# Performance work log

Measured on AMD Instinct MI355X. Metric: run time of the kernel, lower is better.

The kernel has to match this reference:

```python
import jax, jax.numpy as jnp
import numpy as np

EPS_BN = 1e-5


def _batchnorm(h, g, b):
    # training-mode BatchNorm1d over the flattened (B*N*k) axis
    mu = jnp.mean(h, axis=0)
    var = jnp.var(h, axis=0)
    return g * (h - mu) * jax.lax.rsqrt(var + EPS_BN) + b


def setup_inputs() -> dict:
    key = jax.random.key(0)
    ks = jax.random.split(key, 5)
    B, N = 4, 8192
    x = jax.random.normal(ks[0], (B, N, 3), dtype=jnp.float32)
    W1 = jax.random.normal(ks[1], (7, 10), dtype=jnp.float32) * (1.0 / np.sqrt(7.0))
    b1 = jax.random.normal(ks[2], (10,), dtype=jnp.float32) * 0.01
    W2 = jax.random.normal(ks[3], (10, 10), dtype=jnp.float32) * (1.0 / np.sqrt(10.0))
    b2 = jax.random.normal(ks[4], (10,), dtype=jnp.float32) * 0.01
    g1 = jnp.ones((10,), jnp.float32); be1 = jnp.zeros((10,), jnp.float32)
    g2 = jnp.ones((10,), jnp.float32); be2 = jnp.zeros((10,), jnp.float32)
    return {"x": x, "W1": W1, "b1": b1, "g1": g1, "be1": be1,
            "W2": W2, "b2": b2, "g2": g2, "be2": be2, "k": 9}


def reference(x, W1, b1, g1, be1, W2, b2, g2, be2, k):
    B, N, C = x.shape
    # --- kNN graph (brute force, self included as nearest) ---
    sq = jnp.sum(x * x, axis=-1)                                    # (B,N)
    d2 = sq[:, :, None] + sq[:, None, :] - 2.0 * jnp.einsum('bnc,bmc->bnm', x, x)
    _, idx = jax.lax.top_k(-d2, k + 1)                              # (B,N,k+1)
    nbrs = x[jnp.arange(B)[:, None, None], idx]                     # (B,N,k+1,3)
    rel = (nbrs - x[:, :, None, :])[:, :, 1:, :]                    # drop self -> (B,N,k,3)
    # --- sort neighbors by azimuth phi = atan2(y, x) ---
    phi = jnp.arctan2(rel[..., 1], rel[..., 0])                     # (B,N,k)
    order = jnp.argsort(phi, axis=-1)
    v1 = jnp.take_along_axis(rel, order[..., None], axis=2)         # (B,N,k,3)
    v2 = jnp.roll(v1, -1, axis=2)                                   # next neighbor (cyclic)
    # --- umbrella-style surface features ---
    centroids = 0.5 * (v1 + v2)
    normals = jnp.cross(v1, v2)
    normals = normals / (jnp.linalg.norm(normals, axis=-1, keepdims=True) + 1e-6)
    sign = jnp.where(normals[..., 0:1, 0] > 0, 1.0, -1.0)[..., None]  # (B,N,1,1)
    normals = normals * sign
    position = jnp.sum(normals * centroids, axis=-1, keepdims=True) / jnp.sqrt(jnp.asarray(3.0, x.dtype))
    feat = jnp.concatenate([centroids, normals, position], axis=-1)   # (B,N,k,7)
    feat = feat.reshape(B * N * k, 7)
    # --- tiny MLP + max-pool over k ---
    h = jax.nn.relu(_batchnorm(feat @ W1 + b1, g1, be1))
    h = jax.nn.relu(_batchnorm(h @ W2 + b2, g2, be2))
    return jnp.max(h.reshape(B, N, k, 10), axis=2)                  # (B,N,10)
```

## Files before the change

kernel.cpp:

```cpp
#include <hip/hip_runtime.h>
#include <math.h>
#include <float.h>
#include <stdint.h>

#define B_ 4
#define N_ 8192
#define K_ 9
#define NPTS (B_ * N_)
#define NROWS (NPTS * K_)
#define SPLIT 8
#define CHUNK (N_ / SPLIT)
#define NGROUP 32
#define GSIZE (CHUNK / NGROUP)
#define GSTRIDE 33
#define NCOPY 16

typedef float f4 __attribute__((ext_vector_type(4)));
typedef float f32x2 __attribute__((ext_vector_type(2)));

__device__ __forceinline__ f32x2 dist2_pk(f32x2 xx, f32x2 yy, f32x2 zz, f32x2 ww,
                                          f32x2 qx, f32x2 qy, f32x2 qz, f32x2 qw) {
  f32x2 t0 = qx * xx;
  f32x2 t1 = __builtin_elementwise_fma(qy, yy, t0);
  f32x2 t2 = __builtin_elementwise_fma(qz, zz, t1);
  f32x2 s  = qw + ww;
  f32x2 m2 = {-2.0f, -2.0f};
  return __builtin_elementwise_fma(t2, m2, s);
}

#define GDECL(G) float gd##G; int gi##G;
#define TOURN8()                                                           \
  float e01d, e23d, e45d, e67d, f03d, f47d, md;                            \
  int   e01i, e23i, e45i, e67i, f03i, f47i, mi;                            \
  { bool t;                                                                \
    t = d1 < d0; e01d = t ? d1 : d0; e01i = t ? (j + 1) : (j + 0);         \
    t = d3 < d2; e23d = t ? d3 : d2; e23i = t ? (j + 3) : (j + 2);         \
    t = d5 < d4; e45d = t ? d5 : d4; e45i = t ? (j + 5) : (j + 4);         \
    t = d7 < d6; e67d = t ? d7 : d6; e67i = t ? (j + 7) : (j + 6);         \
    t = e23d < e01d; f03d = t ? e23d : e01d; f03i = t ? e23i : e01i;       \
    t = e67d < e45d; f47d = t ? e67d : e45d; f47i = t ? e67i : e45i;       \
    t = f47d < f03d; md = t ? f47d : f03d; mi = t ? f47i : f03i; }
#define SCANG(G)                                                           \
  { float bgd = FLT_MAX; int bgi = 0;                                      \
    _Pragma("clang loop unroll(disable)")                                  \
    for (int pr = 0; pr < 16; pr += 4) {                                   \
      const f4* cp = CH + (G * GSTRIDE + 2 * pr);                          \
      f4 A0 = cp[0], B0 = cp[1], A1 = cp[2], B1 = cp[3];                   \
      f4 A2 = cp[4], B2 = cp[5], A3 = cp[6], B3 = cp[7];                   \
      int j = G * GSIZE + 2 * pr;                                          \
      f32x2 dA = dist2_pk(__builtin_shufflevector(A0, A0, 0, 1),           \
                          __builtin_shufflevector(A0, A0, 2, 3),           \
                          __builtin_shufflevector(B0, B0, 0, 1),           \
                          __builtin_shufflevector(B0, B0, 2, 3),           \
                          qx2, qy2, qz2, qw2);                             \
      f32x2 dB = dist2_pk(__builtin_shufflevector(A1, A1, 0, 1),           \
                          __builtin_shufflevector(A1, A1, 2, 3),           \
                          __builtin_shufflevector(B1, B1, 0, 1),           \
                          __builtin_shufflevector(B1, B1, 2, 3),           \
                          qx2, qy2, qz2, qw2);                             \
      f32x2 dC = dist2_pk(__builtin_shufflevector(A2, A2, 0, 1),           \
                          __builtin_shufflevector(A2, A2, 2, 3),           \
                          __builtin_shufflevector(B2, B2, 0, 1),           \
                          __builtin_shufflevector(B2, B2, 2, 3),           \
                          qx2, qy2, qz2, qw2);                             \
      f32x2 dD = dist2_pk(__builtin_shufflevector(A3, A3, 0, 1),           \
                          __builtin_shufflevector(A3, A3, 2, 3),           \
                          __builtin_shufflevector(B3, B3, 0, 1),           \
                          __builtin_shufflevector(B3, B3, 2, 3),           \
                          qx2, qy2, qz2, qw2);                             \
      float d0 = dA.x, d1 = dA.y, d2 = dB.x, d3 = dB.y;                    \
      float d4 = dC.x, d5 = dC.y, d6 = dD.x, d7 = dD.y;                    \
      if (HS) {                                                            \
        d0 = (j + 0 == nl) ? FLT_MAX : d0;                                 \
        d1 = (j + 1 == nl) ? FLT_MAX : d1;                                 \
        d2 = (j + 2 == nl) ? FLT_MAX : d2;                                 \
        d3 = (j + 3 == nl) ? FLT_MAX : d3;                                 \
        d4 = (j + 4 == nl) ? FLT_MAX : d4;                                 \
        d5 = (j + 5 == nl) ? FLT_MAX : d5;                                 \
        d6 = (j + 6 == nl) ? FLT_MAX : d6;                                 \
        d7 = (j + 7 == nl) ? FLT_MAX : d7;                                 \
      }                                                                    \
      TOURN8();                                                            \
      bool lt = md < bgd; bgd = lt ? md : bgd; bgi = lt ? mi : bgi;        \
    }                                                                      \
    gd##G = bgd; gi##G = bgi; }
#define LMC(G, S)                                                          \
  { bool lt = gd##G < wd##S;                                               \
    wd##S = lt ? gd##G : wd##S; wi##S = lt ? gi##G : wi##S;                \
    wg##S = lt ? G : wg##S; }
#define CMB(S)                                                             \
  { bool lt = wd##S < wda;                                                 \
    wda = lt ? wd##S : wda; wia = lt ? wi##S : wia; wga = lt ? wg##S : wga; }
#define WBK(G)                                                             \
  { bool m = (wg == G); gd##G = m ? nd : gd##G; gi##G = m ? ni : gi##G; }

template <bool HS>
__device__ __forceinline__ void knn_chunk(const f4* CH, f32x2 qx2, f32x2 qy2,
                                          f32x2 qz2, f32x2 qw2,
                                          int nl, int j0, int s, int p,
                                          uint2* __restrict__ PBDI) {
  GDECL(0) GDECL(1) GDECL(2) GDECL(3) GDECL(4) GDECL(5) GDECL(6) GDECL(7)
  GDECL(8) GDECL(9) GDECL(10) GDECL(11) GDECL(12) GDECL(13) GDECL(14) GDECL(15)
  GDECL(16) GDECL(17) GDECL(18) GDECL(19) GDECL(20) GDECL(21) GDECL(22) GDECL(23)
  GDECL(24) GDECL(25) GDECL(26) GDECL(27) GDECL(28) GDECL(29) GDECL(30) GDECL(31)

  SCANG(0) SCANG(1) SCANG(2) SCANG(3) SCANG(4) SCANG(5) SCANG(6) SCANG(7)
  SCANG(8) SCANG(9) SCANG(10) SCANG(11) SCANG(12) SCANG(13) SCANG(14) SCANG(15)
  SCANG(16) SCANG(17) SCANG(18) SCANG(19) SCANG(20) SCANG(21) SCANG(22) SCANG(23)
  SCANG(24) SCANG(25) SCANG(26) SCANG(27) SCANG(28) SCANG(29) SCANG(30) SCANG(31)

#pragma clang loop unroll(disable)
  for (int r = 0; r < K_; ++r) {
    float wda = gd0; int wia = gi0; int wga = 0;
    LMC(1,a) LMC(2,a) LMC(3,a) LMC(4,a) LMC(5,a) LMC(6,a) LMC(7,a)
    float wdb = gd8; int wib = gi8; int wgb = 8;
    LMC(9,b) LMC(10,b) LMC(11,b) LMC(12,b) LMC(13,b) LMC(14,b) LMC(15,b)
    float wdc = gd16; int wic = gi16; int wgc = 16;
    LMC(17,c) LMC(18,c) LMC(19,c) LMC(20,c) LMC(21,c) LMC(22,c) LMC(23,c)
    float wdd = gd24; int wid = gi24; int wgd = 24;
    LMC(25,d) LMC(26,d) LMC(27,d) LMC(28,d) LMC(29,d) LMC(30,d) LMC(31,d)
    CMB(b) CMB(c) CMB(d)
    float wd = wda; int wi = wia; int wg = wga;

    uint2 o; o.x = __float_as_uint(wd); o.y = (unsigned)(j0 + wi);
    PBDI[(size_t)(s * K_ + r) * NPTS + p] = o;

    int ab = wg * GSTRIDE;
    int jb = wg * GSIZE;
    float nd = FLT_MAX; int ni = 0;
#pragma clang loop unroll(disable)
    for (int pr = 0; pr < 16; pr += 4) {
      const f4* cp = CH + (ab + 2 * pr);
      f4 A0 = cp[0], B0 = cp[1], A1 = cp[2], B1 = cp[3];
      f4 A2 = cp[4], B2 = cp[5], A3 = cp[6], B3 = cp[7];
      int j = jb + 2 * pr;
      f32x2 dA = dist2_pk(__builtin_shufflevector(A0, A0, 0, 1),
                          __builtin_shufflevector(A0, A0, 2, 3),
                          __builtin_shufflevector(B0, B0, 0, 1),
                          __builtin_shufflevector(B0, B0, 2, 3),
                          qx2, qy2, qz2, qw2);
      f32x2 dB = dist2_pk(__builtin_shufflevector(A1, A1, 0, 1),
                          __builtin_shufflevector(A1, A1, 2, 3),
                          __builtin_shufflevector(B1, B1, 0, 1),
                          __builtin_shufflevector(B1, B1, 2, 3),
                          qx2, qy2, qz2, qw2);
      f32x2 dC = dist2_pk(__builtin_shufflevector(A2, A2, 0, 1),
                          __builtin_shufflevector(A2, A2, 2, 3),
                          __builtin_shufflevector(B2, B2, 0, 1),
                          __builtin_shufflevector(B2, B2, 2, 3),
                          qx2, qy2, qz2, qw2);
      f32x2 dD = dist2_pk(__builtin_shufflevector(A3, A3, 0, 1),
                          __builtin_shufflevector(A3, A3, 2, 3),
                          __builtin_shufflevector(B3, B3, 0, 1),
                          __builtin_shufflevector(B3, B3, 2, 3),
                          qx2, qy2, qz2, qw2);
      float d0 = dA.x, d1 = dA.y, d2 = dB.x, d3 = dB.y;
      float d4 = dC.x, d5 = dC.y, d6 = dD.x, d7 = dD.y;
      if (HS) {
        d0 = (j + 0 == nl) ? FLT_MAX : d0;
        d1 = (j + 1 == nl) ? FLT_MAX : d1;
        d2 = (j + 2 == nl) ? FLT_MAX : d2;
        d3 = (j + 3 == nl) ? FLT_MAX : d3;
        d4 = (j + 4 == nl) ? FLT_MAX : d4;
        d5 = (j + 5 == nl) ? FLT_MAX : d5;
        d6 = (j + 6 == nl) ? FLT_MAX : d6;
        d7 = (j + 7 == nl) ? FLT_MAX : d7;
      }
      bool k0 = (d0 > wd) | ((d0 == wd) & ((j + 0) > wi));
      bool k1 = (d1 > wd) | ((d1 == wd) & ((j + 1) > wi));
      bool k2 = (d2 > wd) | ((d2 == wd) & ((j + 2) > wi));
      bool k3 = (d3 > wd) | ((d3 == wd) & ((j + 3) > wi));
      bool k4 = (d4 > wd) | ((d4 == wd) & ((j + 4) > wi));
      bool k5 = (d5 > wd) | ((d5 == wd) & ((j + 5) > wi));
      bool k6 = (d6 > wd) | ((d6 == wd) & ((j + 6) > wi));
      bool k7 = (d7 > wd) | ((d7 == wd) & ((j + 7) > wi));
      d0 = k0 ? d0 : FLT_MAX;
      d1 = k1 ? d1 : FLT_MAX;
      d2 = k2 ? d2 : FLT_MAX;
      d3 = k3 ? d3 : FLT_MAX;
      d4 = k4 ? d4 : FLT_MAX;
      d5 = k5 ? d5 : FLT_MAX;
      d6 = k6 ? d6 : FLT_MAX;
      d7 = k7 ? d7 : FLT_MAX;
      TOURN8();
      bool lt = md < nd; nd = lt ? md : nd; ni = lt ? mi : ni;
    }
    WBK(0) WBK(1) WBK(2) WBK(3) WBK(4) WBK(5) WBK(6) WBK(7)
    WBK(8) WBK(9) WBK(10) WBK(11) WBK(12) WBK(13) WBK(14) WBK(15)
    WBK(16) WBK(17) WBK(18) WBK(19) WBK(20) WBK(21) WBK(22) WBK(23)
    WBK(24) WBK(25) WBK(26) WBK(27) WBK(28) WBK(29) WBK(30) WBK(31)
  }
}

__launch_bounds__(128, 4)
__global__ void k_knn(const float* __restrict__ x, uint2* __restrict__ PBDI) {
  __shared__ f4 CH[NGROUP * GSTRIDE];
  int bid = blockIdx.x;
  int pg = bid >> 3;
  int s = bid & (SPLIT - 1);
  int p = pg * 128 + threadIdx.x;
  int b = p >> 13;
  int n = p & (N_ - 1);
  int bO = b * N_;
  int j0 = s * CHUNK;

  const float* xq = x + 3 * (size_t)p;
  float qa = xq[0], qb = xq[1], qc = xq[2];
  float qw = qa * qa + qb * qb + qc * qc;
  f32x2 qx2 = {qa, qa}, qy2 = {qb, qb}, qz2 = {qc, qc}, qw2 = {qw, qw};

  for (int u = threadIdx.x; u < CHUNK / 2; u += 128) {
    const float* xp = x + 3 * (size_t)(bO + j0 + 2 * u);
    float a0 = xp[0], b0 = xp[1], c0 = xp[2];
    float a1 = xp[3], b1 = xp[4], c1 = xp[5];
    int G = u >> 4, rr = u & 15;
    f4 lo = {a0, a1, b0, b1};
    f4 hi = {c0, c1, a0 * a0 + b0 * b0 + c0 * c0, a1 * a1 + b1 * b1 + c1 * c1};
    CH[G * GSTRIDE + 2 * rr] = lo;
    CH[G * GSTRIDE + 2 * rr + 1] = hi;
  }
  __syncthreads();

  int n0 = (pg * 128) & (N_ - 1);
  int nl = n - j0;
  if (s == (n0 >> 10)) knn_chunk<true >(CH, qx2, qy2, qz2, qw2, nl, j0, s, p, PBDI);
  else                 knn_chunk<false>(CH, qx2, qy2, qz2, qw2, nl, j0, s, p, PBDI);
}

#define LVL(bdv, biv)                                                     \
  { bool lt = cd < (bdv); float td = (bdv); int ti = (biv);               \
    (bdv) = lt ? cd : (bdv); (biv) = lt ? ci : (biv);                     \
    cd = lt ? td : cd; ci = lt ? ti : ci; }
#define INS9ALL()                                                         \
  LVL(b0d, b0i) LVL(b1d, b1i) LVL(b2d, b2i) LVL(b3d, b3i) LVL(b4d, b4i)  \
  LVL(b5d, b5i) LVL(b6d, b6i) LVL(b7d, b7i) LVL(b8d, b8i)
#define TOP9_DECL()                                                       \
  float b0d = FLT_MAX, b1d = FLT_MAX, b2d = FLT_MAX, b3d = FLT_MAX,       \
        b4d = FLT_MAX, b5d = FLT_MAX, b6d = FLT_MAX, b7d = FLT_MAX,       \
        b8d = FLT_MAX;                                                    \
  int b0i = 0, b1i = 0, b2i = 0, b3i = 0, b4i = 0, b5i = 0, b6i = 0,      \
      b7i = 0, b8i = 0;

#define MKREL(T)                                                          \
  float rx##T, ry##T, rz##T, ph##T;                                       \
  { const float* mp = x + 3 * (size_t)(bO + b##T##i);                     \
    rx##T = mp[0] - qa; ry##T = mp[1] - qb; rz##T = mp[2] - qc;           \
    ph##T = atan2f(ry##T, rx##T); }

#define CE(A, Bv)                                                         \
  { bool lt = ph##Bv < ph##A; float t0;                                   \
    t0 = ph##A; ph##A = lt ? ph##Bv : t0; ph##Bv = lt ? t0 : ph##Bv;      \
    t0 = rx##A; rx##A = lt ? rx##Bv : t0; rx##Bv = lt ? t0 : rx##Bv;      \
    t0 = ry##A; ry##A = lt ? ry##Bv : t0; ry##Bv = lt ? t0 : ry##Bv;      \
    t0 = rz##A; rz##A = lt ? rz##Bv : t0; rz##Bv = lt ? t0 : rz##Bv; }

#define ST9(arr, v0, v1, v2, v3, v4, v5, v6, v7, v8)                      \
  arr[0 * 64 + pl] = v0; arr[1 * 64 + pl] = v1; arr[2 * 64 + pl] = v2;    \
  arr[3 * 64 + pl] = v3; arr[4 * 64 + pl] = v4; arr[5 * 64 + pl] = v5;    \
  arr[6 * 64 + pl] = v6; arr[7 * 64 + pl] = v7; arr[8 * 64 + pl] = v8;

__launch_bounds__(256, 4)
__global__ void k_tail1(const float* __restrict__ x, const uint2* __restrict__ PBDI,
                        const float* __restrict__ W1, const float* __restrict__ b1,
                        float* __restrict__ H1, double* __restrict__ ACC) {
  __shared__ float  LMD[64 * 37];
  __shared__ int    LMI[64 * 37];
  __shared__ float  LREL[3][9 * 64];
  __shared__ float  LSGN[64];
  __shared__ double sred[4][20];

  int q = threadIdx.x >> 6;
  int pl = threadIdx.x & 63;
  int pbase = blockIdx.x * 64;
  int p = pbase + pl;

  {
    TOP9_DECL();
#pragma clang loop unroll_count(2)
    for (int e = 0; e < 2 * K_; ++e) {
      uint2 v = PBDI[(size_t)(q * 2 * K_ + e) * NPTS + p];
      float cd = __uint_as_float(v.x);
      int ci = (int)v.y;
      INS9ALL();
    }
    int base = pl * 37 + q * 9;
    LMD[base + 0] = b0d; LMD[base + 1] = b1d; LMD[base + 2] = b2d;
    LMD[base + 3] = b3d; LMD[base + 4] = b4d; LMD[base + 5] = b5d;
    LMD[base + 6] = b6d; LMD[base + 7] = b7d; LMD[base + 8] = b8d;
    LMI[base + 0] = b0i; LMI[base + 1] = b1i; LMI[base + 2] = b2i;
    LMI[base + 3] = b3i; LMI[base + 4] = b4i; LMI[base + 5] = b5i;
    LMI[base + 6] = b6i; LMI[base + 7] = b7i; LMI[base + 8] = b8i;
  }
  __syncthreads();

  if (q == 0) {
    int b = p >> 13;
    int bO = b * N_;
    const float* xq = x + 3 * (size_t)p;
    float qa = xq[0], qb = xq[1], qc = xq[2];

    TOP9_DECL();
#pragma clang loop unroll_count(3)
    for (int e = 0; e < 4 * K_; ++e) {
      float cd = LMD[pl * 37 + e];
      int ci = LMI[pl * 37 + e];
      INS9ALL();
    }

    MKREL(0) MKREL(1) MKREL(2) MKREL(3) MKREL(4)
    MKREL(5) MKREL(6) MKREL(7) MKREL(8)

    CE(0,1)
    CE(1,2) CE(0,1)
    CE(2,3) CE(1,2) CE(0,1)
    CE(3,4) CE(2,3) CE(1,2) CE(0,1)
    CE(4,5) CE(3,4) CE(2,3) CE(1,2) CE(0,1)
    CE(5,6) CE(4,5) CE(3,4) CE(2,3) CE(1,2) CE(0,1)
    CE(6,7) CE(5,6) CE(4,5) CE(3,4) CE(2,3) CE(1,2) CE(0,1)
    CE(7,8) CE(6,7) CE(5,6) CE(4,5) CE(3,4) CE(2,3) CE(1,2) CE(0,1)

    float nx0 = ry0 * rz1 - rz0 * ry1;
    float ny0 = rz0 * rx1 - rx0 * rz1;
    float nz0 = rx0 * ry1 - ry0 * rx1;
    float nrm0 = sqrtf(nx0 * nx0 + ny0 * ny0 + nz0 * nz0) + 1e-6f;
    LSGN[pl] = ((nx0 / nrm0) > 0.0f) ? 1.0f : -1.0f;

    ST9(LREL[0], rx0, rx1, rx2, rx3, rx4, rx5, rx6, rx7, rx8)
    ST9(LREL[1], ry0, ry1, ry2, ry3, ry4, ry5, ry6, ry7, ry8)
    ST9(LREL[2], rz0, rz1, rz2, rz3, rz4, rz5, rz6, rz7, rz8)
  }
  __syncthreads();

  double sum[10], ss[10];
#pragma unroll
  for (int c = 0; c < 10; ++c) { sum[c] = 0.0; ss[c] = 0.0; }

#pragma clang loop unroll(disable)
  for (int rl = threadIdx.x; rl < 9 * 64; rl += 256) {
    int t = rl >> 6;
    int pp = rl & 63;
    int t2 = (t + 1 == K_) ? 0 : t + 1;
    float v1x = LREL[0][t * 64 + pp];
    float v1y = LREL[1][t * 64 + pp];
    float v1z = LREL[2][t * 64 + pp];
    float v2x = LREL[0][t2 * 64 + pp];
    float v2y = LREL[1][t2 * 64 + pp];
    float v2z = LREL[2][t2 * 64 + pp];
    float sgn = LSGN[pp];

    float cx = 0.5f * (v1x + v2x);
    float cy = 0.5f * (v1y + v2y);
    float cz = 0.5f * (v1z + v2z);
    float nx = v1y * v2z - v1z * v2y;
    float ny = v1z * v2x - v1x * v2z;
    float nz = v1x * v2y - v1y * v2x;
    float nrm = sqrtf(nx * nx + ny * ny + nz * nz) + 1e-6f;
    nx /= nrm; ny /= nrm; nz /= nrm;
    nx *= sgn; ny *= sgn; nz *= sgn;
    float pos = (nx * cx + ny * cy + nz * cz) / 1.7320508075688772f;

    float fv[7] = {cx, cy, cz, nx, ny, nz, pos};
#pragma unroll
    for (int c = 0; c < 10; ++c) {
      float h = b1[c];
#pragma unroll
      for (int rr = 0; rr < 7; ++rr) h = fmaf(fv[rr], W1[rr * 10 + c], h);
      H1[(size_t)c * NROWS + (size_t)t * NPTS + pbase + pp] = h;
      double hd = (double)h;
      sum[c] += hd; ss[c] += hd * hd;
    }
  }

  int lane = threadIdx.x & 63, wv = threadIdx.x >> 6;
#pragma unroll
  for (int c = 0; c < 10; ++c) {
    double a = sum[c];
#pragma unroll
    for (int off = 32; off > 0; off >>= 1) a += __shfl_down(a, off);
    if (lane == 0) sred[wv][c] = a;
    double qq = ss[c];
#pragma unroll
    for (int off = 32; off > 0; off >>= 1) qq += __shfl_down(qq, off);
    if (lane == 0) sred[wv][10 + c] = qq;
  }
  __syncthreads();
  if (threadIdx.x < 20) {
    atomicAdd(&ACC[(blockIdx.x & (NCOPY - 1)) * 40 + threadIdx.x],
              sred[0][threadIdx.x] + sred[1][threadIdx.x] +
              sred[2][threadIdx.x] + sred[3][threadIdx.x]);
  }
}

__launch_bounds__(64)
__global__ void k_mlp2(const float* __restrict__ H1, double* __restrict__ ACC,
                       const float* __restrict__ g1, const float* __restrict__ be1,
                       const float* __restrict__ W2, const float* __restrict__ b2,
                       const float* __restrict__ g2, float* __restrict__ EXT) {
  __shared__ float MR[20];
  __shared__ double sred[20];
  if (threadIdx.x < 20) {
    int c = threadIdx.x % 10;
    int half = threadIdx.x / 10;
    double s0 = 0.0, s1 = 0.0;
#pragma unroll
    for (int cc = 0; cc < NCOPY; ++cc) {
      s0 += ACC[cc * 40 + c];
      s1 += ACC[cc * 40 + 10 + c];
    }
    double mu = s0 / (double)NROWS;
    double var = s1 / (double)NROWS - mu * mu;
    MR[threadIdx.x] = half ? (float)(1.0 / sqrt(var + 1e-5)) : (float)mu;
  }
  __syncthreads();

  int p = blockIdx.x * 64 + threadIdx.x;
  double sum[10], ss[10];
  float ext[10], sg[10];
#pragma unroll
  for (int c = 0; c < 10; ++c) {
    sum[c] = 0.0; ss[c] = 0.0;
    sg[c] = g2[c];
    ext[c] = (sg[c] >= 0.0f) ? -FLT_MAX : FLT_MAX;
  }

#pragma clang loop unroll(disable)
  for (int t = 0; t < K_; ++t) {
    float v[10];
#pragma unroll
    for (int c = 0; c < 10; ++c) {
      float h = H1[(size_t)c * NROWS + (size_t)t * NPTS + p];
      float z = g1[c] * (h - MR[c]) * MR[10 + c] + be1[c];
      v[c] = z > 0.0f ? z : 0.0f;
    }
#pragma unroll
    for (int c = 0; c < 10; ++c) {
      float h = b2[c];
#pragma unroll
      for (int u = 0; u < 10; ++u) h = fmaf(v[u], W2[u * 10 + c], h);
      sum[c] += (double)h;
      ss[c] += (double)h * (double)h;
      ext[c] = (sg[c] >= 0.0f) ? fmaxf(ext[c], h) : fminf(ext[c], h);
    }
  }

#pragma unroll
  for (int c = 0; c < 10; ++c)
    EXT[(size_t)c * NPTS + p] = ext[c];

#pragma unroll
  for (int c = 0; c < 10; ++c) {
    double a = sum[c];
#pragma unroll
    for (int off = 32; off > 0; off >>= 1) a += __shfl_down(a, off);
    if (threadIdx.x == 0) sred[c] = a;
    double qq = ss[c];
#pragma unroll
    for (int off = 32; off > 0; off >>= 1) qq += __shfl_down(qq, off);
    if (threadIdx.x == 0) sred[10 + c] = qq;
  }
  __syncthreads();
  if (threadIdx.x < 20) {
    atomicAdd(&ACC[(blockIdx.x & (NCOPY - 1)) * 40 + 20 + threadIdx.x],
              sred[threadIdx.x]);
  }
}

__launch_bounds__(64)
__global__ void k_out(const float* __restrict__ EXT, const double* __restrict__ ACC,
                      const float* __restrict__ g2, const float* __restrict__ be2,
                      float* __restrict__ out) {
  __shared__ float MR[20];
  if (threadIdx.x < 20) {
    int c = threadIdx.x % 10;
    int half = threadIdx.x / 10;
    double s0 = 0.0, s1 = 0.0;
#pragma unroll
    for (int cc = 0; cc < NCOPY; ++cc) {
      s0 += ACC[cc * 40 + 20 + c];
      s1 += ACC[cc * 40 + 30 + c];
    }
    double mu = s0 / (double)NROWS;
    double var = s1 / (double)NROWS - mu * mu;
    MR[threadIdx.x] = half ? (float)(1.0 / sqrt(var + 1e-5)) : (float)mu;
  }
  __syncthreads();

  int p = blockIdx.x * 64 + threadIdx.x;
#pragma unroll
  for (int c = 0; c < 10; ++c) {
    float h = EXT[(size_t)c * NPTS + p];
    float z = g2[c] * (h - MR[c]) * MR[10 + c] + be2[c];
    z = z > 0.0f ? z : 0.0f;
    out[(size_t)p * 10 + c] = z;
  }
}

extern "C" void kernel_launch(void* const* d_in, const int* in_sizes, int n_in,
                              void* d_out, int out_size, void* d_ws, size_t ws_size,
                              hipStream_t stream) {
  (void)in_sizes; (void)n_in; (void)out_size; (void)ws_size;
  const float* x  = (const float*)d_in[0];
  const float* W1 = (const float*)d_in[1];
  const float* b1 = (const float*)d_in[2];
  const float* g1 = (const float*)d_in[3];
  const float* be1= (const float*)d_in[4];
  const float* W2 = (const float*)d_in[5];
  const float* b2 = (const float*)d_in[6];
  const float* g2 = (const float*)d_in[7];
  const float* be2= (const float*)d_in[8];
  float* out = (float*)d_out;

  char* base = (char*)d_ws;
  uint2*  PBDI = (uint2*)base;
  float*  H1 = (float*)(base + (size_t)SPLIT * K_ * NPTS * 8);
  double* ACC = (double*)(H1 + (size_t)10 * NROWS);
  float*  EXT = (float*)PBDI;

  hipMemsetAsync(ACC, 0, NCOPY * 40 * sizeof(double), stream);
  k_knn<<<(NPTS / 128) * SPLIT, 128, 0, stream>>>(x, PBDI);
  k_tail1<<<NPTS / 64, 256, 0, stream>>>(x, PBDI, W1, b1, H1, ACC);
  k_mlp2<<<NPTS / 64, 64, 0, stream>>>(H1, ACC, g1, be1, W2, b2, g2, EXT);
  k_out<<<NPTS / 64, 64, 0, stream>>>(EXT, ACC, g2, be2, out);
}
```

Measured before the change: 231.6 us.

## Process two query points per thread in kNN scan and defer index recovery

Each thread now handles two query points, so every LDS load of candidate points is reused for two distance computations. The initial per-group scan keeps only the min distance and which 8-wide sub-block held it, using fminf. The exact index is recovered lazily during extraction by recomputing that sub-block. The ACC memset is folded into block 0 of the kNN kernel, and launch bounds drop to 2 waves/SIMD, which raises register pressure and halves the grid size.

```diff
diff --git a/kernel.cpp b/kernel.cpp
--- a/kernel.cpp
+++ b/kernel.cpp
@@ -18,6 +18,8 @@
 typedef float f4 __attribute__((ext_vector_type(4)));
 typedef float f32x2 __attribute__((ext_vector_type(2)));
 
+#define SH2(V, a, b) __builtin_shufflevector(V, V, a, b)
+
 __device__ __forceinline__ f32x2 dist2_pk(f32x2 xx, f32x2 yy, f32x2 zz, f32x2 ww,
                                           f32x2 qx, f32x2 qy, f32x2 qz, f32x2 qw) {
   f32x2 t0 = qx * xx;
@@ -28,7 +30,69 @@
   return __builtin_elementwise_fma(t2, m2, s);
 }
 
-#define GDECL(G) float gd##G; int gi##G;
+#define WLOAD(cp)                                                          \
+  f4 A0 = (cp)[0], B0 = (cp)[1], A1 = (cp)[2], B1 = (cp)[3],               \
+     A2 = (cp)[4], B2 = (cp)[5], A3 = (cp)[6], B3 = (cp)[7];
+
+#define WDIST(QX, QY, QZ, QW)                                              \
+  f32x2 dP0 = dist2_pk(SH2(A0,0,1), SH2(A0,2,3), SH2(B0,0,1), SH2(B0,2,3), \
+                       QX, QY, QZ, QW);                                    \
+  f32x2 dP1 = dist2_pk(SH2(A1,0,1), SH2(A1,2,3), SH2(B1,0,1), SH2(B1,2,3), \
+                       QX, QY, QZ, QW);                                    \
+  f32x2 dP2 = dist2_pk(SH2(A2,0,1), SH2(A2,2,3), SH2(B2,0,1), SH2(B2,2,3), \
+                       QX, QY, QZ, QW);                                    \
+  f32x2 dP3 = dist2_pk(SH2(A3,0,1), SH2(A3,2,3), SH2(B3,0,1), SH2(B3,2,3), \
+                       QX, QY, QZ, QW);                                    \
+  float d0 = dP0.x, d1 = dP0.y, d2 = dP1.x, d3 = dP1.y;                    \
+  float d4 = dP2.x, d5 = dP2.y, d6 = dP3.x, d7 = dP3.y;
+
+#define HSMASK(JV, NL)                                                     \
+  if (HS) {                                                                \
+    d0 = ((JV) + 0 == (NL)) ? FLT_MAX : d0;                                \
+    d1 = ((JV) + 1 == (NL)) ? FLT_MAX : d1;                                \
+    d2 = ((JV) + 2 == (NL)) ? FLT_MAX : d2;                                \
+    d3 = ((JV) + 3 == (NL)) ? FLT_MAX : d3;                                \
+    d4 = ((JV) + 4 == (NL)) ? FLT_MAX : d4;                                \
+    d5 = ((JV) + 5 == (NL)) ? FLT_MAX : d5;                                \
+    d6 = ((JV) + 6 == (NL)) ? FLT_MAX : d6;                                \
+    d7 = ((JV) + 7 == (NL)) ? FLT_MAX : d7;                                \
+  }
+
+#define FMIN8 fminf(fminf(fminf(d0, d1), fminf(d2, d3)),                   \
+                    fminf(fminf(d4, d5), fminf(d6, d7)))
+
+#define GDECL2(G) float gdA##G; int giA##G; float gdB##G; int giB##G;
+
+#define SCANG2(G)                                                          \
+  { float bgdA = FLT_MAX; int bqA = 0;                                     \
+    float bgdB = FLT_MAX; int bqB = 0;                                     \
+    _Pragma("clang loop unroll(disable)")                                  \
+    for (int pr = 0; pr < 16; pr += 4) {                                   \
+      const f4* cp = CH + (G * GSTRIDE + 2 * pr);                          \
+      WLOAD(cp)                                                            \
+      int j = G * GSIZE + 2 * pr;                                          \
+      { WDIST(qx2A, qy2A, qz2A, qw2A)                                      \
+        HSMASK(j, nlA)                                                     \
+        float m = FMIN8;                                                   \
+        bool lt = m < bgdA; bgdA = lt ? m : bgdA; bqA = lt ? pr : bqA; }   \
+      { WDIST(qx2B, qy2B, qz2B, qw2B)                                      \
+        HSMASK(j, nlB)                                                     \
+        float m = FMIN8;                                                   \
+        bool lt = m < bgdB; bgdB = lt ? m : bgdB; bqB = lt ? pr : bqB; }   \
+    }                                                                      \
+    gdA##G = bgdA; giA##G = -1 - bqA;                                      \
+    gdB##G = bgdB; giB##G = -1 - bqB; }
+
+#define LMQ(G, S, Q)                                                       \
+  { bool lt = gd##Q##G < wd##S;                                            \
+    wd##S = lt ? gd##Q##G : wd##S; wi##S = lt ? gi##Q##G : wi##S;          \
+    wg##S = lt ? G : wg##S; }
+#define CMBQ(S)                                                            \
+  { bool lt = wd##S < wda;                                                 \
+    wda = lt ? wd##S : wda; wia = lt ? wi##S : wia; wga = lt ? wg##S : wga; }
+#define WBKQ(G, Q)                                                         \
+  { bool m = (wg == G); gd##Q##G = m ? nd : gd##Q##G;                      \
+    gi##Q##G = m ? ni : gi##Q##G; }
 #define TOURN8()                                                           \
   float e01d, e23d, e45d, e67d, f03d, f47d, md;                            \
   int   e01i, e23i, e45i, e67i, f03i, f47i, mi;                            \
@@ -40,174 +104,143 @@
     t = e23d < e01d; f03d = t ? e23d : e01d; f03i = t ? e23i : e01i;       \
     t = e67d < e45d; f47d = t ? e67d : e45d; f47i = t ? e67i : e45i;       \
     t = f47d < f03d; md = t ? f47d : f03d; mi = t ? f47i : f03i; }
-#define SCANG(G)                                                           \
-  { float bgd = FLT_MAX; int bgi = 0;                                      \
+
+#define EXTRACTLOOP(Q)                                                     \
+  _Pragma("clang loop unroll(disable)")                                    \
+  for (int r = 0; r < K_; ++r) {                                           \
+    float wda = gd##Q##0; int wia = gi##Q##0; int wga = 0;                 \
+    LMQ(1,a,Q) LMQ(2,a,Q) LMQ(3,a,Q) LMQ(4,a,Q) LMQ(5,a,Q) LMQ(6,a,Q)     \
+    LMQ(7,a,Q)                                                             \
+    float wdb = gd##Q##8; int wib = gi##Q##8; int wgb = 8;                 \
+    LMQ(9,b,Q) LMQ(10,b,Q) LMQ(11,b,Q) LMQ(12,b,Q) LMQ(13,b,Q)            \
+    LMQ(14,b,Q) LMQ(15,b,Q)                                                \
+    float wdc = gd##Q##16; int wic = gi##Q##16; int wgc = 16;              \
+    LMQ(17,c,Q) LMQ(18,c,Q) LMQ(19,c,Q) LMQ(20,c,Q) LMQ(21,c,Q)           \
+    LMQ(22,c,Q) LMQ(23,c,Q)                                                \
+    float wdd = gd##Q##24; int wid = gi##Q##24; int wgd = 24;              \
+    LMQ(25,d,Q) LMQ(26,d,Q) LMQ(27,d,Q) LMQ(28,d,Q) LMQ(29,d,Q)           \
+    LMQ(30,d,Q) LMQ(31,d,Q)                                                \
+    CMBQ(b) CMBQ(c) CMBQ(d)                                                \
+    float wd = wda; int wist = wia; int wg = wga;                          \
+    int ab = wg * GSTRIDE;                                                 \
+    int jb = wg * GSIZE;                                                   \
+    int wi;                                                                \
+    { int bq = (wist >= 0) ? 0 : (-1 - wist);                              \
+      const f4* cp = CH + (ab + 2 * bq);                                   \
+      WLOAD(cp)                                                            \
+      int j = jb + 2 * bq;                                                 \
+      WDIST(qx2, qy2, qz2, qw2)                                            \
+      HSMASK(j, nl)                                                        \
+      const int IMX = 0x7fffffff;                                          \
+      int a0_ = (d0 == wd) ? (j + 0) : IMX;                                \
+      int a1_ = (d1 == wd) ? (j + 1) : IMX;                                \
+      int a2_ = (d2 == wd) ? (j + 2) : IMX;                                \
+      int a3_ = (d3 == wd) ? (j + 3) : IMX;                                \
+      int a4_ = (d4 == wd) ? (j + 4) : IMX;                                \
+      int a5_ = (d5 == wd) ? (j + 5) : IMX;                                \
+      int a6_ = (d6 == wd) ? (j + 6) : IMX;                                \
+      int a7_ = (d7 == wd) ? (j + 7) : IMX;                                \
+      int m01 = a0_ < a1_ ? a0_ : a1_;                                     \
+      int m23 = a2_ < a3_ ? a2_ : a3_;                                     \
+      int m45 = a4_ < a5_ ? a4_ : a5_;                                     \
+      int m67 = a6_ < a7_ ? a6_ : a7_;                                     \
+      int mA_ = m01 < m23 ? m01 : m23;                                     \
+      int mB_ = m45 < m67 ? m45 : m67;                                     \
+      int jm = mA_ < mB_ ? mA_ : mB_;                                      \
+      wi = (wist >= 0) ? wist : jm; }                                      \
+    uint2 o; o.x = __float_as_uint(wd); o.y = (unsigned)(j0 + wi);         \
+    PBDI[(size_t)(s * K_ + r) * NPTS + p] = o;                             \
+    float nd = FLT_MAX; int ni = 0;                                        \
     _Pragma("clang loop unroll(disable)")                                  \
     for (int pr = 0; pr < 16; pr += 4) {                                   \
-      const f4* cp = CH + (G * GSTRIDE + 2 * pr);                          \
-      f4 A0 = cp[0], B0 = cp[1], A1 = cp[2], B1 = cp[3];                   \
-      f4 A2 = cp[4], B2 = cp[5], A3 = cp[6], B3 = cp[7];                   \
-      int j = G * GSIZE + 2 * pr;                                          \
-      f32x2 dA = dist2_pk(__builtin_shufflevector(A0, A0, 0, 1),           \
-                          __builtin_shufflevector(A0, A0, 2, 3),           \
-                          __builtin_shufflevector(B0, B0, 0, 1),           \
-                          __builtin_shufflevector(B0, B0, 2, 3),           \
-                          qx2, qy2, qz2, qw2);                             \
-      f32x2 dB = dist2_pk(__builtin_shufflevector(A1, A1, 0, 1),           \
-                          __builtin_shufflevector(A1, A1, 2, 3),           \
-                          __builtin_shufflevector(B1, B1, 0, 1),           \
-                          __builtin_shufflevector(B1, B1, 2, 3),           \
-                          qx2, qy2, qz2, qw2);                             \
-      f32x2 dC = dist2_pk(__builtin_shufflevector(A2, A2, 0, 1),           \
-                          __builtin_shufflevector(A2, A2, 2, 3),           \
-                          __builtin_shufflevector(B2, B2, 0, 1),           \
-                          __builtin_shufflevector(B2, B2, 2, 3),           \
-                          qx2, qy2, qz2, qw2);                             \
-      f32x2 dD = dist2_pk(__builtin_shufflevector(A3, A3, 0, 1),           \
-                          __builtin_shufflevector(A3, A3, 2, 3),           \
-                          __builtin_shufflevector(B3, B3, 0, 1),           \
-                          __builtin_shufflevector(B3, B3, 2, 3),           \
-                          qx2, qy2, qz2, qw2);                             \
-      float d0 = dA.x, d1 = dA.y, d2 = dB.x, d3 = dB.y;                    \
-      float d4 = dC.x, d5 = dC.y, d6 = dD.x, d7 = dD.y;                    \
-      if (HS) {                                                            \
-        d0 = (j + 0 == nl) ? FLT_MAX : d0;                                 \
-        d1 = (j + 1 == nl) ? FLT_MAX : d1;                                 \
-        d2 = (j + 2 == nl) ? FLT_MAX : d2;                                 \
-        d3 = (j + 3 == nl) ? FLT_MAX : d3;                                 \
-        d4 = (j + 4 == nl) ? FLT_MAX : d4;                                 \
-        d5 = (j + 5 == nl) ? FLT_MAX : d5;                                 \
-        d6 = (j + 6 == nl) ? FLT_MAX : d6;                                 \
-        d7 = (j + 7 == nl) ? FLT_MAX : d7;                                 \
-      }                                                                    \
+      const f4* cp = CH + (ab + 2 * pr);                                   \
+      WLOAD(cp)                                                            \
+      int j = jb + 2 * pr;                                                 \
+      WDIST(qx2, qy2, qz2, qw2)                                            \
+      HSMASK(j, nl)                                                        \
+      bool k0 = (d0 > wd) | ((d0 == wd) & ((j + 0) > wi));                 \
+      bool k1 = (d1 > wd) | ((d1 == wd) & ((j + 1) > wi));                 \
+      bool k2 = (d2 > wd) | ((d2 == wd) & ((j + 2) > wi));                 \
+      bool k3 = (d3 > wd) | ((d3 == wd) & ((j + 3) > wi));                 \
+      bool k4 = (d4 > wd) | ((d4 == wd) & ((j + 4) > wi));                 \
+      bool k5 = (d5 > wd) | ((d5 == wd) & ((j + 5) > wi));                 \
+      bool k6 = (d6 > wd) | ((d6 == wd) & ((j + 6) > wi));                 \
+      bool k7 = (d7 > wd) | ((d7 == wd) & ((j + 7) > wi));                 \
+      d0 = k0 ? d0 : FLT_MAX;                                              \
+      d1 = k1 ? d1 : FLT_MAX;                                              \
+      d2 = k2 ? d2 : FLT_MAX;                                              \
+      d3 = k3 ? d3 : FLT_MAX;                                              \
+      d4 = k4 ? d4 : FLT_MAX;                                              \
+      d5 = k5 ? d5 : FLT_MAX;                                              \
+      d6 = k6 ? d6 : FLT_MAX;                                              \
+      d7 = k7 ? d7 : FLT_MAX;                                              \
       TOURN8();                                                            \
-      bool lt = md < bgd; bgd = lt ? md : bgd; bgi = lt ? mi : bgi;        \
+      bool lt = md < nd; nd = lt ? md : nd; ni = lt ? mi : ni;             \
     }                                                                      \
-    gd##G = bgd; gi##G = bgi; }
-#define LMC(G, S)                                                          \
-  { bool lt = gd##G < wd##S;                                               \
-    wd##S = lt ? gd##G : wd##S; wi##S = lt ? gi##G : wi##S;                \
-    wg##S = lt ? G : wg##S; }
-#define CMB(S)                                                             \
-  { bool lt = wd##S < wda;                                                 \
-    wda = lt ? wd##S : wda; wia = lt ? wi##S : wia; wga = lt ? wg##S : wga; }
-#define WBK(G)                                                             \
-  { bool m = (wg == G); gd##G = m ? nd : gd##G; gi##G = m ? ni : gi##G; }
+    WBKQ(0,Q) WBKQ(1,Q) WBKQ(2,Q) WBKQ(3,Q) WBKQ(4,Q) WBKQ(5,Q)           \
+    WBKQ(6,Q) WBKQ(7,Q) WBKQ(8,Q) WBKQ(9,Q) WBKQ(10,Q) WBKQ(11,Q)         \
+    WBKQ(12,Q) WBKQ(13,Q) WBKQ(14,Q) WBKQ(15,Q) WBKQ(16,Q) WBKQ(17,Q)     \
+    WBKQ(18,Q) WBKQ(19,Q) WBKQ(20,Q) WBKQ(21,Q) WBKQ(22,Q) WBKQ(23,Q)     \
+    WBKQ(24,Q) WBKQ(25,Q) WBKQ(26,Q) WBKQ(27,Q) WBKQ(28,Q) WBKQ(29,Q)     \
+    WBKQ(30,Q) WBKQ(31,Q)                                                  \
+  }
 
 template <bool HS>
-__device__ __forceinline__ void knn_chunk(const f4* CH, f32x2 qx2, f32x2 qy2,
-                                          f32x2 qz2, f32x2 qw2,
-                                          int nl, int j0, int s, int p,
-                                          uint2* __restrict__ PBDI) {
-  GDECL(0) GDECL(1) GDECL(2) GDECL(3) GDECL(4) GDECL(5) GDECL(6) GDECL(7)
-  GDECL(8) GDECL(9) GDECL(10) GDECL(11) GDECL(12) GDECL(13) GDECL(14) GDECL(15)
-  GDECL(16) GDECL(17) GDECL(18) GDECL(19) GDECL(20) GDECL(21) GDECL(22) GDECL(23)
-  GDECL(24) GDECL(25) GDECL(26) GDECL(27) GDECL(28) GDECL(29) GDECL(30) GDECL(31)
-
-  SCANG(0) SCANG(1) SCANG(2) SCANG(3) SCANG(4) SCANG(5) SCANG(6) SCANG(7)
-  SCANG(8) SCANG(9) SCANG(10) SCANG(11) SCANG(12) SCANG(13) SCANG(14) SCANG(15)
-  SCANG(16) SCANG(17) SCANG(18) SCANG(19) SCANG(20) SCANG(21) SCANG(22) SCANG(23)
-  SCANG(24) SCANG(25) SCANG(26) SCANG(27) SCANG(28) SCANG(29) SCANG(30) SCANG(31)
-
-#pragma clang loop unroll(disable)
-  for (int r = 0; r < K_; ++r) {
-    float wda = gd0; int wia = gi0; int wga = 0;
-    LMC(1,a) LMC(2,a) LMC(3,a) LMC(4,a) LMC(5,a) LMC(6,a) LMC(7,a)
-    float wdb = gd8; int wib = gi8; int wgb = 8;
-    LMC(9,b) LMC(10,b) LMC(11,b) LMC(12,b) LMC(13,b) LMC(14,b) LMC(15,b)
-    float wdc = gd16; int wic = gi16; int wgc = 16;
-    LMC(17,c) LMC(18,c) LMC(19,c) LMC(20,c) LMC(21,c) LMC(22,c) LMC(23,c)
-    float wdd = gd24; int wid = gi24; int wgd = 24;
-    LMC(25,d) LMC(26,d) LMC(27,d) LMC(28,d) LMC(29,d) LMC(30,d) LMC(31,d)
-    CMB(b) CMB(c) CMB(d)
-    float wd = wda; int wi = wia; int wg = wga;
-
-    uint2 o; o.x = __float_as_uint(wd); o.y = (unsigned)(j0 + wi);
-    PBDI[(size_t)(s * K_ + r) * NPTS + p] = o;
-
-    int ab = wg * GSTRIDE;
-    int jb = wg * GSIZE;
-    float nd = FLT_MAX; int ni = 0;
-#pragma clang loop unroll(disable)
-    for (int pr = 0; pr < 16; pr += 4) {
-      const f4* cp = CH + (ab + 2 * pr);
-      f4 A0 = cp[0], B0 = cp[1], A1 = cp[2], B1 = cp[3];
-      f4 A2 = cp[4], B2 = cp[5], A3 = cp[6], B3 = cp[7];
-      int j = jb + 2 * pr;
-      f32x2 dA = dist2_pk(__builtin_shufflevector(A0, A0, 0, 1),
-                          __builtin_shufflevector(A0, A0, 2, 3),
-                          __builtin_shufflevector(B0, B0, 0, 1),
-                          __builtin_shufflevector(B0, B0, 2, 3),
-                          qx2, qy2, qz2, qw2);
-      f32x2 dB = dist2_pk(__builtin_shufflevector(A1, A1, 0, 1),
-                          __builtin_shufflevector(A1, A1, 2, 3),
-                          __builtin_shufflevector(B1, B1, 0, 1),
-                          __builtin_shufflevector(B1, B1, 2, 3),
-                          qx2, qy2, qz2, qw2);
-      f32x2 dC = dist2_pk(__builtin_shufflevector(A2, A2, 0, 1),
-                          __builtin_shufflevector(A2, A2, 2, 3),
-                          __builtin_shufflevector(B2, B2, 0, 1),
-                          __builtin_shufflevector(B2, B2, 2, 3),
-                          qx2, qy2, qz2, qw2);
-      f32x2 dD = dist2_pk(__builtin_shufflevector(A3, A3, 0, 1),
-                          __builtin_shufflevector(A3, A3, 2, 3),
-                          __builtin_shufflevector(B3, B3, 0, 1),
-                          __builtin_shufflevector(B3, B3, 2, 3),
-                          qx2, qy2, qz2, qw2);
-      float d0 = dA.x, d1 = dA.y, d2 = dB.x, d3 = dB.y;
-      float d4 = dC.x, d5 = dC.y, d6 = dD.x, d7 = dD.y;
-      if (HS) {
-        d0 = (j + 0 == nl) ? FLT_MAX : d0;
-        d1 = (j + 1 == nl) ? FLT_MAX : d1;
-        d2 = (j + 2 == nl) ? FLT_MAX : d2;
-        d3 = (j + 3 == nl) ? FLT_MAX : d3;
-        d4 = (j + 4 == nl) ? FLT_MAX : d4;
-        d5 = (j + 5 == nl) ? FLT_MAX : d5;
-        d6 = (j + 6 == nl) ? FLT_MAX : d6;
-        d7 = (j + 7 == nl) ? FLT_MAX : d7;
-      }
-      bool k0 = (d0 > wd) | ((d0 == wd) & ((j + 0) > wi));
-      bool k1 = (d1 > wd) | ((d1 == wd) & ((j + 1) > wi));
-      bool k2 = (d2 > wd) | ((d2 == wd) & ((j + 2) > wi));
-      bool k3 = (d3 > wd) | ((d3 == wd) & ((j + 3) > wi));
-      bool k4 = (d4 > wd) | ((d4 == wd) & ((j + 4) > wi));
-      bool k5 = (d5 > wd) | ((d5 == wd) & ((j + 5) > wi));
-      bool k6 = (d6 > wd) | ((d6 == wd) & ((j + 6) > wi));
-      bool k7 = (d7 > wd) | ((d7 == wd) & ((j + 7) > wi));
-      d0 = k0 ? d0 : FLT_MAX;
-      d1 = k1 ? d1 : FLT_MAX;
-      d2 = k2 ? d2 : FLT_MAX;
-      d3 = k3 ? d3 : FLT_MAX;
-      d4 = k4 ? d4 : FLT_MAX;
-      d5 = k5 ? d5 : FLT_MAX;
-      d6 = k6 ? d6 : FLT_MAX;
-      d7 = k7 ? d7 : FLT_MAX;
-      TOURN8();
-      bool lt = md < nd; nd = lt ? md : nd; ni = lt ? mi : ni;
-    }
-    WBK(0) WBK(1) WBK(2) WBK(3) WBK(4) WBK(5) WBK(6) WBK(7)
-    WBK(8) WBK(9) WBK(10) WBK(11) WBK(12) WBK(13) WBK(14) WBK(15)
-    WBK(16) WBK(17) WBK(18) WBK(19) WBK(20) WBK(21) WBK(22) WBK(23)
-    WBK(24) WBK(25) WBK(26) WBK(27) WBK(28) WBK(29) WBK(30) WBK(31)
-  }
-}
-
-__launch_bounds__(128, 4)
-__global__ void k_knn(const float* __restrict__ x, uint2* __restrict__ PBDI) {
+__device__ __forceinline__ void knn_chunk2(
+    const f4* CH,
+    f32x2 qx2A, f32x2 qy2A, f32x2 qz2A, f32x2 qw2A,
+    f32x2 qx2B, f32x2 qy2B, f32x2 qz2B, f32x2 qw2B,
+    int nlA, int nlB, int j0, int s, int p0, int p1,
+    uint2* __restrict__ PBDI) {
+  GDECL2(0) GDECL2(1) GDECL2(2) GDECL2(3) GDECL2(4) GDECL2(5) GDECL2(6)
+  GDECL2(7) GDECL2(8) GDECL2(9) GDECL2(10) GDECL2(11) GDECL2(12) GDECL2(13)
+  GDECL2(14) GDECL2(15) GDECL2(16) GDECL2(17) GDECL2(18) GDECL2(19)
+  GDECL2(20) GDECL2(21) GDECL2(22) GDECL2(23) GDECL2(24) GDECL2(25)
+  GDECL2(26) GDECL2(27) GDECL2(28) GDECL2(29) GDECL2(30) GDECL2(31)
+
+  SCANG2(0) SCANG2(1) SCANG2(2) SCANG2(3) SCANG2(4) SCANG2(5) SCANG2(6)
+  SCANG2(7) SCANG2(8) SCANG2(9) SCANG2(10) SCANG2(11) SCANG2(12) SCANG2(13)
+  SCANG2(14) SCANG2(15) SCANG2(16) SCANG2(17) SCANG2(18) SCANG2(19)
+  SCANG2(20) SCANG2(21) SCANG2(22) SCANG2(23) SCANG2(24) SCANG2(25)
+  SCANG2(26) SCANG2(27) SCANG2(28) SCANG2(29) SCANG2(30) SCANG2(31)
+
+  {
+    f32x2 qx2 = qx2A, qy2 = qy2A, qz2 = qz2A, qw2 = qw2A;
+    int nl = nlA; int p = p0;
+    EXTRACTLOOP(A)
+  }
+  {
+    f32x2 qx2 = qx2B, qy2 = qy2B, qz2 = qz2B, qw2 = qw2B;
+    int nl = nlB; int p = p1;
+    EXTRACTLOOP(B)
+  }
+}
+
+__launch_bounds__(128, 2)
+__global__ void k_knn(const float* __restrict__ x, uint2* __restrict__ PBDI,
+                      double* __restrict__ ACC) {
   __shared__ f4 CH[NGROUP * GSTRIDE];
   int bid = blockIdx.x;
+  if (bid == 0) {
+    for (int t = threadIdx.x; t < NCOPY * 40; t += 128) ACC[t] = 0.0;
+  }
   int pg = bid >> 3;
   int s = bid & (SPLIT - 1);
-  int p = pg * 128 + threadIdx.x;
-  int b = p >> 13;
-  int n = p & (N_ - 1);
+  int pbase = pg * 256;
+  int p0 = pbase + threadIdx.x;
+  int p1 = p0 + 128;
+  int b = p0 >> 13;
   int bO = b * N_;
   int j0 = s * CHUNK;
 
-  const float* xq = x + 3 * (size_t)p;
-  float qa = xq[0], qb = xq[1], qc = xq[2];
-  float qw = qa * qa + qb * qb + qc * qc;
-  f32x2 qx2 = {qa, qa}, qy2 = {qb, qb}, qz2 = {qc, qc}, qw2 = {qw, qw};
+  const float* xq0 = x + 3 * (size_t)p0;
+  float qa0 = xq0[0], qb0 = xq0[1], qc0 = xq0[2];
+  float qw0 = qa0 * qa0 + qb0 * qb0 + qc0 * qc0;
+  const float* xq1 = x + 3 * (size_t)p1;
+  float qa1 = xq1[0], qb1 = xq1[1], qc1 = xq1[2];
+  float qw1 = qa1 * qa1 + qb1 * qb1 + qc1 * qc1;
+  f32x2 qx2A = {qa0, qa0}, qy2A = {qb0, qb0}, qz2A = {qc0, qc0}, qw2A = {qw0, qw0};
+  f32x2 qx2B = {qa1, qa1}, qy2B = {qb1, qb1}, qz2B = {qc1, qc1}, qw2B = {qw1, qw1};
 
   for (int u = threadIdx.x; u < CHUNK / 2; u += 128) {
     const float* xp = x + 3 * (size_t)(bO + j0 + 2 * u);
@@ -221,10 +254,15 @@
   }
   __syncthreads();
 
-  int n0 = (pg * 128) & (N_ - 1);
-  int nl = n - j0;
-  if (s == (n0 >> 10)) knn_chunk<true >(CH, qx2, qy2, qz2, qw2, nl, j0, s, p, PBDI);
-  else                 knn_chunk<false>(CH, qx2, qy2, qz2, qw2, nl, j0, s, p, PBDI);
+  int n0 = pbase & (N_ - 1);
+  int nlA = (n0 + threadIdx.x) - j0;
+  int nlB = nlA + 128;
+  if (s == (n0 >> 10))
+    knn_chunk2<true >(CH, qx2A, qy2A, qz2A, qw2A, qx2B, qy2B, qz2B, qw2B,
+                      nlA, nlB, j0, s, p0, p1, PBDI);
+  else
+    knn_chunk2<false>(CH, qx2A, qy2A, qz2A, qw2A, qx2B, qy2B, qz2B, qw2B,
+                      nlA, nlB, j0, s, p0, p1, PBDI);
 }
 
 #define LVL(bdv, biv)                                                     \
@@ -516,8 +554,7 @@
   double* ACC = (double*)(H1 + (size_t)10 * NROWS);
   float*  EXT = (float*)PBDI;
 
-  hipMemsetAsync(ACC, 0, NCOPY * 40 * sizeof(double), stream);
-  k_knn<<<(NPTS / 128) * SPLIT, 128, 0, stream>>>(x, PBDI);
+  k_knn<<<(NPTS / 256) * SPLIT, 128, 0, stream>>>(x, PBDI, ACC);
   k_tail1<<<NPTS / 64, 256, 0, stream>>>(x, PBDI, W1, b1, H1, ACC);
   k_mlp2<<<NPTS / 64, 64, 0, stream>>>(H1, ACC, g1, be1, W2, b2, g2, EXT);
   k_out<<<NPTS / 64, 64, 0, stream>>>(EXT, ACC, g2, be2, out);
```

Result: faster. 226.0 us (-2.4%).
